# Optimization experiments

Measured on AMD Instinct MI355X. Metric: run time of the kernel, lower is better.

The kernel has to match this reference:

```python
import jax, jax.numpy as jnp
import numpy as np

EPS = 1e-5  # torch LayerNorm default


def _layernorm_hd(t, gamma, beta):
    # Normalize jointly over the last two axes (n_heads, head_dim),
    # matching nn.LayerNorm((n_heads, head_dim)).
    mu = jnp.mean(t, axis=(-2, -1), keepdims=True)
    var = jnp.var(t, axis=(-2, -1), keepdims=True)
    return (t - mu) * jax.lax.rsqrt(var + EPS) * gamma + beta


def setup_inputs() -> dict:
    key = jax.random.key(0)
    B, Hs, Ws, C = 4, 256, 256, 128  # batch, spatial grid, hidden_channels
    n_heads, head_dim = 4, C // 4
    scale = (C ** 2) / n_heads  # hidden_channels**2 / n_heads, as in __init__
    ks = jax.random.split(key, 4)
    X = jax.random.normal(ks[0], (B, Hs, Ws, C), dtype=jnp.float32)
    Wq = jax.random.normal(ks[1], (C, n_heads, head_dim), dtype=jnp.float32) / scale
    Wk = jax.random.normal(ks[2], (C, n_heads, head_dim), dtype=jnp.float32) / scale
    Wv = jax.random.normal(ks[3], (C, n_heads, head_dim), dtype=jnp.float32) / scale
    # NOTE: original forward applies layernorm_key to BOTH key and value
    # (layernorm_value params are unused); we replicate that exactly.
    gamma_k = jnp.ones((n_heads, head_dim), dtype=jnp.float32)
    beta_k = jnp.zeros((n_heads, head_dim), dtype=jnp.float32)
    return {"X": X, "Wq": Wq, "Wk": Wk, "Wv": Wv, "gamma_k": gamma_k, "beta_k": beta_k}


def reference(X, Wq, Wk, Wv, gamma_k, beta_k):
    # X: [B, Hs, Ws, C]; W*: [C, h, d]
    q = jnp.einsum('bxyc,chd->bxyhd', X, Wq)
    k = jnp.einsum('bxyc,chd->bxyhd', X, Wk)
    v = jnp.einsum('bxyc,chd->bxyhd', X, Wv)
    k = _layernorm_hd(k, gamma_k, beta_k)
    v = _layernorm_hd(v, gamma_k, beta_k)  # faithful: layernorm_key used for value too
    num_points = X.shape[1] * X.shape[2]
    kv = jnp.einsum('bxyhd,bxyhe->bhde', k, v)          # tiny [B,h,d,d]
    sa = jnp.einsum('bxyhd,bhde->bxyeh', q, kv)          # note output order (e, h)
    sa = (sa / num_points).reshape(X.shape)
    return sa
```

## Files before the change

kernel.cpp:

```cpp
#include <hip/hip_runtime.h>

#define HW 65536
#define CH 128
#define NHEADS 4
#define HDIM 32
#define EPS 1e-5f
#define INV_NP (1.0f / 65536.0f)
#define INV_C (1.0f / 128.0f)

typedef float v4f __attribute__((ext_vector_type(4)));
typedef short v8s __attribute__((ext_vector_type(8)));
typedef unsigned int v2u __attribute__((ext_vector_type(2)));
typedef unsigned int v4u __attribute__((ext_vector_type(4)));

__device__ __forceinline__ ushort f2bf(float f) {
    uint u = __float_as_uint(f);
    return (ushort)((u + 0x7FFFu + ((u >> 16) & 1u)) >> 16);
}

#define MFMA(a, b, c) __builtin_amdgcn_mfma_f32_16x16x32_bf16((a), (b), (c), 0, 0, 0)

#define LDS_WKT 0
#define LDS_WVT 16384
#define LDS_XS  32768
#define LDS_KST 32768
#define LDS_VST 36864

__global__ __launch_bounds__(256, 2) void kv_kernel(const float* __restrict__ X,
                                                    const float* __restrict__ Wk,
                                                    const float* __restrict__ Wv,
                                                    const float* __restrict__ gamma,
                                                    const float* __restrict__ beta,
                                                    float* __restrict__ kv_g) {
    __shared__ ushort lds[40960];
    const int tid  = threadIdx.x;
    const int lane = tid & 63;
    const int w    = tid >> 6;
    const int q    = lane >> 4;
    const int ln   = lane & 15;
    const int phalf = w >> 1;
    const int isv   = w & 1;
    const int WTb   = isv ? LDS_WVT : LDS_WKT;

    const int batch  = blockIdx.x >> 7;
    const int blocal = blockIdx.x & 127;
    const float* Xb = X + ((size_t)batch * HW + (size_t)blocal * 512) * CH;

#pragma unroll
    for (int n = 0; n < 16; ++n) {
        const int idx = n * 256 + tid;
        const int c  = idx >> 5;
        const int j0 = (idx & 31) << 2;
        const float4 a = ((const float4*)Wk)[idx];
        const float4 b = ((const float4*)Wv)[idx];
        const int cb = (c >> 5) * 4096 + (c & 31);
        lds[LDS_WKT + cb + (j0 + 0) * 32] = f2bf(a.x);
        lds[LDS_WKT + cb + (j0 + 1) * 32] = f2bf(a.y);
        lds[LDS_WKT + cb + (j0 + 2) * 32] = f2bf(a.z);
        lds[LDS_WKT + cb + (j0 + 3) * 32] = f2bf(a.w);
        lds[LDS_WVT + cb + (j0 + 0) * 32] = f2bf(b.x);
        lds[LDS_WVT + cb + (j0 + 1) * 32] = f2bf(b.y);
        lds[LDS_WVT + cb + (j0 + 2) * 32] = f2bf(b.z);
        lds[LDS_WVT + cb + (j0 + 3) * 32] = f2bf(b.w);
    }

    float g8[8], be8[8];
#pragma unroll
    for (int ct = 0; ct < 8; ++ct) {
        g8[ct]  = gamma[ct * 16 + ln];
        be8[ct] = beta[ct * 16 + ln];
    }

    v4f kv00 = {0.f, 0.f, 0.f, 0.f}, kv01 = kv00, kv10 = kv00, kv11 = kv00;

    float4 xp[8];
#pragma unroll
    for (int n = 0; n < 8; ++n) xp[n] = ((const float4*)Xb)[n * 256 + tid];

    for (int t = 0; t < 8; ++t) {
        __syncthreads();
#pragma unroll
        for (int n = 0; n < 8; ++n) {
            const int idx = n * 256 + tid;
            const int p  = idx >> 5;
            const int c0 = (idx & 31) << 2;
            const int off = LDS_XS + ((c0 >> 5) << 11) + (p << 5) + (c0 & 31);
            v2u pk;
            pk.x = (uint)f2bf(xp[n].x) | ((uint)f2bf(xp[n].y) << 16);
            pk.y = (uint)f2bf(xp[n].z) | ((uint)f2bf(xp[n].w) << 16);
            *(v2u*)(lds + off) = pk;
        }
        if (t < 7) {
            const float4* src = (const float4*)(Xb + (size_t)(t + 1) * 64 * CH);
#pragma unroll
            for (int n = 0; n < 8; ++n) xp[n] = src[n * 256 + tid];
        }
        __syncthreads();

        v4f acc[2][8];
#pragma unroll
        for (int rt = 0; rt < 2; ++rt)
#pragma unroll
            for (int ct = 0; ct < 8; ++ct) acc[rt][ct] = kv00 * 0.f;
#pragma unroll
        for (int ks = 0; ks < 4; ++ks) {
            const v8s A0 = *(const v8s*)(lds + LDS_XS + ks * 2048 + (phalf * 32 + ln) * 32 + q * 8);
            const v8s A1 = *(const v8s*)(lds + LDS_XS + ks * 2048 + (phalf * 32 + 16 + ln) * 32 + q * 8);
#pragma unroll
            for (int ct = 0; ct < 8; ++ct) {
                const v8s B = *(const v8s*)(lds + WTb + ks * 4096 + (ct * 16 + ln) * 32 + q * 8);
                acc[0][ct] = MFMA(A0, B, acc[0][ct]);
                acc[1][ct] = MFMA(A1, B, acc[1][ct]);
            }
        }

        float mu[2][4], rs[2][4];
#pragma unroll
        for (int rt = 0; rt < 2; ++rt) {
#pragma unroll
            for (int r = 0; r < 4; ++r) {
                float s = 0.f, sq = 0.f;
#pragma unroll
                for (int ct = 0; ct < 8; ++ct) {
                    const float v = acc[rt][ct][r];
                    s += v;
                    sq += v * v;
                }
#pragma unroll
                for (int m = 1; m <= 8; m <<= 1) {
                    s  += __shfl_xor(s, m);
                    sq += __shfl_xor(sq, m);
                }
                const float m1 = s * INV_C;
                const float var = sq * INV_C - m1 * m1;
                mu[rt][r] = m1;
                rs[rt][r] = 1.0f / sqrtf(var + EPS);
            }
        }

        __syncthreads();

#pragma unroll
        for (int rnd = 0; rnd < 2; ++rnd) {
            if (phalf == rnd) {
                const int base = (isv ? LDS_VST : LDS_KST);
#pragma unroll
                for (int ct = 0; ct < 8; ++ct) {
                    const int chb = base + (ct * 16 + ln) * 32;
#pragma unroll
                    for (int rt = 0; rt < 2; ++rt) {
#pragma unroll
                        for (int r = 0; r < 4; r += 2) {
                            const float v0 = (acc[rt][ct][r] - mu[rt][r]) * rs[rt][r] * g8[ct] + be8[ct];
                            const float v1 = (acc[rt][ct][r + 1] - mu[rt][r + 1]) * rs[rt][r + 1] * g8[ct] + be8[ct];
                            const int p32 = rt * 16 + q * 4 + r;
                            *(uint*)(lds + chb + p32) = (uint)f2bf(v0) | ((uint)f2bf(v1) << 16);
                        }
                    }
                }
            }
            __syncthreads();
            {
                const v8s Ad0 = *(const v8s*)(lds + LDS_KST + (w * 32 + ln) * 32 + q * 8);
                const v8s Ad1 = *(const v8s*)(lds + LDS_KST + (w * 32 + 16 + ln) * 32 + q * 8);
                const v8s Be0 = *(const v8s*)(lds + LDS_VST + (w * 32 + ln) * 32 + q * 8);
                const v8s Be1 = *(const v8s*)(lds + LDS_VST + (w * 32 + 16 + ln) * 32 + q * 8);
                kv00 = MFMA(Ad0, Be0, kv00);
                kv01 = MFMA(Ad0, Be1, kv01);
                kv10 = MFMA(Ad1, Be0, kv10);
                kv11 = MFMA(Ad1, Be1, kv11);
            }
            __syncthreads();
        }
    }

    float* dst = kv_g + (batch * NHEADS + w) * (HDIM * HDIM);
#pragma unroll
    for (int dt = 0; dt < 2; ++dt)
#pragma unroll
        for (int et = 0; et < 2; ++et) {
            const v4f f = dt == 0 ? (et == 0 ? kv00 : kv01) : (et == 0 ? kv10 : kv11);
#pragma unroll
            for (int r = 0; r < 4; ++r) {
                const int d = dt * 16 + q * 4 + r;
                const int e = et * 16 + ln;
                atomicAdd(&dst[d * HDIM + e], f[r]);
            }
        }
}

__global__ __launch_bounds__(256) void weff_kernel(const float* __restrict__ Wq,
                                                   const float* __restrict__ kv_g,
                                                   ushort* __restrict__ WeffT) {
    const int b = blockIdx.x >> 4;
    const int part = blockIdx.x & 15;
    const int base = part * 1024 + threadIdx.x * 4;
    const int c = base >> 7;
    const int o0 = base & 127;
    const float* kvb = kv_g + b * (NHEADS * HDIM * HDIM);
#pragma unroll
    for (int n = 0; n < 4; ++n) {
        const int o = o0 + n;
        const int h = o & 3;
        const int e = o >> 2;
        float s = 0.f;
#pragma unroll
        for (int d = 0; d < HDIM; ++d)
            s += Wq[c * CH + h * HDIM + d] * kvb[h * (HDIM * HDIM) + d * HDIM + e];
        WeffT[b * (CH * CH) + o * CH + c] = f2bf(s * INV_NP);
    }
}

__global__ __launch_bounds__(256, 2) void out_kernel(const float* __restrict__ X,
                                                     const ushort* __restrict__ WeffT,
                                                     float* __restrict__ out) {
    __shared__ ushort lds[32768];
    const int tid  = threadIdx.x;
    const int lane = tid & 63;
    const int w    = tid >> 6;
    const int q    = lane >> 4;
    const int ln   = lane & 15;
    const int phalf = w >> 1;
    const int chalf = w & 1;

    const int batch  = blockIdx.x >> 8;
    const int blocal = blockIdx.x & 255;
    const size_t p0 = (size_t)batch * HW + (size_t)blocal * 256;
    const float* Xb = X + p0 * CH;

    float4 xp[8];
#pragma unroll
    for (int n = 0; n < 8; ++n) xp[n] = ((const float4*)Xb)[n * 256 + tid];

    const ushort* Wt = WeffT + batch * (CH * CH);
#pragma unroll
    for (int n = 0; n < 8; ++n) {
        const int idx = n * 256 + tid;
        const int o  = idx >> 4;
        const int c0 = (idx & 15) << 3;
        const v4u vv = ((const v4u*)Wt)[idx];
        *(v4u*)(lds + (c0 >> 5) * 4096 + o * 32 + (c0 & 31)) = vv;
    }

#pragma unroll
    for (int n = 0; n < 8; ++n) {
        const int idx = n * 256 + tid;
        const int p  = idx >> 5;
        const int c0 = (idx & 31) << 2;
        v2u pk;
        pk.x = (uint)f2bf(xp[n].x) | ((uint)f2bf(xp[n].y) << 16);
        pk.y = (uint)f2bf(xp[n].z) | ((uint)f2bf(xp[n].w) << 16);
        *(v2u*)(lds + 16384 + ((c0 >> 5) << 11) + (p << 5) + (c0 & 31)) = pk;
    }
    __syncthreads();

    for (int t = 0; t < 4; ++t) {
        if (t < 3) {
            const float4* src = (const float4*)(Xb + (size_t)(t + 1) * 64 * CH);
#pragma unroll
            for (int n = 0; n < 8; ++n) xp[n] = src[n * 256 + tid];
        }
        const int xsb = 16384 + (t & 1) * 8192;

        v4f acc[2][4];
#pragma unroll
        for (int rt = 0; rt < 2; ++rt)
#pragma unroll
            for (int ct = 0; ct < 4; ++ct) acc[rt][ct] = (v4f){0.f, 0.f, 0.f, 0.f};
#pragma unroll
        for (int ks = 0; ks < 4; ++ks) {
            const v8s A0 = *(const v8s*)(lds + xsb + ks * 2048 + (phalf * 32 + ln) * 32 + q * 8);
            const v8s A1 = *(const v8s*)(lds + xsb + ks * 2048 + (phalf * 32 + 16 + ln) * 32 + q * 8);
#pragma unroll
            for (int ct = 0; ct < 4; ++ct) {
                const v8s B = *(const v8s*)(lds + ks * 4096 + (chalf * 64 + ct * 16 + ln) * 32 + q * 8);
                acc[0][ct] = MFMA(A0, B, acc[0][ct]);
                acc[1][ct] = MFMA(A1, B, acc[1][ct]);
            }
        }

        if (t < 3) {
            const int xsb2 = 16384 + ((t + 1) & 1) * 8192;
#pragma unroll
            for (int n = 0; n < 8; ++n) {
                const int idx = n * 256 + tid;
                const int p  = idx >> 5;
                const int c0 = (idx & 31) << 2;
                v2u pk;
                pk.x = (uint)f2bf(xp[n].x) | ((uint)f2bf(xp[n].y) << 16);
                pk.y = (uint)f2bf(xp[n].z) | ((uint)f2bf(xp[n].w) << 16);
                *(v2u*)(lds + xsb2 + ((c0 >> 5) << 11) + (p << 5) + (c0 & 31)) = pk;
            }
        }

        float* op = out + (p0 + t * 64) * CH;
#pragma unroll
        for (int rt = 0; rt < 2; ++rt)
#pragma unroll
            for (int ct = 0; ct < 4; ++ct)
#pragma unroll
                for (int r = 0; r < 4; ++r) {
                    const int p = phalf * 32 + rt * 16 + q * 4 + r;
                    const int col = chalf * 64 + ct * 16 + ln;
                    op[p * CH + col] = acc[rt][ct][r];
                }
        __syncthreads();
    }
}

extern "C" void kernel_launch(void* const* d_in, const int* in_sizes, int n_in,
                              void* d_out, int out_size, void* d_ws, size_t ws_size,
                              hipStream_t stream) {
    const float* X     = (const float*)d_in[0];
    const float* Wq    = (const float*)d_in[1];
    const float* Wk    = (const float*)d_in[2];
    const float* Wv    = (const float*)d_in[3];
    const float* gamma = (const float*)d_in[4];
    const float* beta  = (const float*)d_in[5];
    float* out = (float*)d_out;

    float*  kv_g  = (float*)d_ws;
    ushort* WeffT = (ushort*)((char*)d_ws + 65536);

    hipMemsetAsync(kv_g, 0, 16384 * sizeof(float), stream);
    kv_kernel<<<512, 256, 0, stream>>>(X, Wk, Wv, gamma, beta, kv_g);
    weff_kernel<<<64, 256, 0, stream>>>(Wq, kv_g, WeffT);
    out_kernel<<<1024, 256, 0, stream>>>(X, WeffT, out);
}
```

Before: 307.9 us.

## Load X fragments directly into registers, pre-swizzle weights, drop X LDS staging

A new prep kernel converts Wk and Wv to bf16 once, writes them in a swizzled transposed layout, and zeroes the kv accumulator, replacing the memset. The kv and out kernels now copy the pre-swizzled weights into LDS with vector copies and load X straight from global memory into MFMA A-fragments, removing the X LDS staging and several barriers. LDS layouts use XOR-style rotation to avoid bank conflicts, and out_kernel uses smaller blocks without the occupancy hint. In exchange, the explicit register prefetch of the next X tile is gone, so global load latency is now exposed, and the uncoalesced per-lane 32-byte loads may cost bandwidth.

```diff
diff --git a/kernel.cpp b/kernel.cpp
--- a/kernel.cpp
+++ b/kernel.cpp
@@ -10,7 +10,6 @@
 
 typedef float v4f __attribute__((ext_vector_type(4)));
 typedef short v8s __attribute__((ext_vector_type(8)));
-typedef unsigned int v2u __attribute__((ext_vector_type(2)));
 typedef unsigned int v4u __attribute__((ext_vector_type(4)));
 
 __device__ __forceinline__ ushort f2bf(float f) {
@@ -18,17 +17,40 @@
     return (ushort)((u + 0x7FFFu + ((u >> 16) & 1u)) >> 16);
 }
 
+__device__ __forceinline__ v8s pack8(float4 a, float4 b) {
+    v8s r;
+    r[0] = (short)f2bf(a.x); r[1] = (short)f2bf(a.y);
+    r[2] = (short)f2bf(a.z); r[3] = (short)f2bf(a.w);
+    r[4] = (short)f2bf(b.x); r[5] = (short)f2bf(b.y);
+    r[6] = (short)f2bf(b.z); r[7] = (short)f2bf(b.w);
+    return r;
+}
+
 #define MFMA(a, b, c) __builtin_amdgcn_mfma_f32_16x16x32_bf16((a), (b), (c), 0, 0, 0)
 
-#define LDS_WKT 0
-#define LDS_WVT 16384
-#define LDS_XS  32768
-#define LDS_KST 32768
-#define LDS_VST 36864
+
+__global__ __launch_bounds__(256) void prep_kernel(const float* __restrict__ Wk,
+                                                   const float* __restrict__ Wv,
+                                                   ushort* __restrict__ SWkT,
+                                                   ushort* __restrict__ SWvT,
+                                                   float* __restrict__ kv_g) {
+    const int t = blockIdx.x * 256 + threadIdx.x;
+    kv_g[t] = 0.f;
+    kv_g[t + 8192] = 0.f;
+#pragma unroll
+    for (int i = 0; i < 2; ++i) {
+        const int e = i * 8192 + t;
+        const int c = e >> 7;
+        const int row = e & 127;
+        const int dst = row * 128 + (((c >> 3) + row) & 15) * 8 + (c & 7);
+        SWkT[dst] = f2bf(Wk[e]);
+        SWvT[dst] = f2bf(Wv[e]);
+    }
+}
 
 __global__ __launch_bounds__(256, 2) void kv_kernel(const float* __restrict__ X,
-                                                    const float* __restrict__ Wk,
-                                                    const float* __restrict__ Wv,
+                                                    const ushort* __restrict__ SWkT,
+                                                    const ushort* __restrict__ SWvT,
                                                     const float* __restrict__ gamma,
                                                     const float* __restrict__ beta,
                                                     float* __restrict__ kv_g) {
@@ -40,28 +62,22 @@
     const int ln   = lane & 15;
     const int phalf = w >> 1;
     const int isv   = w & 1;
-    const int WTb   = isv ? LDS_WVT : LDS_WKT;
+    const int Wb    = isv ? 16384 : 0;
 
     const int batch  = blockIdx.x >> 7;
     const int blocal = blockIdx.x & 127;
     const float* Xb = X + ((size_t)batch * HW + (size_t)blocal * 512) * CH;
 
-#pragma unroll
-    for (int n = 0; n < 16; ++n) {
-        const int idx = n * 256 + tid;
-        const int c  = idx >> 5;
-        const int j0 = (idx & 31) << 2;
-        const float4 a = ((const float4*)Wk)[idx];
-        const float4 b = ((const float4*)Wv)[idx];
-        const int cb = (c >> 5) * 4096 + (c & 31);
-        lds[LDS_WKT + cb + (j0 + 0) * 32] = f2bf(a.x);
-        lds[LDS_WKT + cb + (j0 + 1) * 32] = f2bf(a.y);
-        lds[LDS_WKT + cb + (j0 + 2) * 32] = f2bf(a.z);
-        lds[LDS_WKT + cb + (j0 + 3) * 32] = f2bf(a.w);
-        lds[LDS_WVT + cb + (j0 + 0) * 32] = f2bf(b.x);
-        lds[LDS_WVT + cb + (j0 + 1) * 32] = f2bf(b.y);
-        lds[LDS_WVT + cb + (j0 + 2) * 32] = f2bf(b.z);
-        lds[LDS_WVT + cb + (j0 + 3) * 32] = f2bf(b.w);
+    {
+        const v4u* sk = (const v4u*)SWkT;
+        const v4u* sv = (const v4u*)SWvT;
+        v4u* dk = (v4u*)lds;
+        v4u* dv = (v4u*)(lds + 16384);
+#pragma unroll
+        for (int n = 0; n < 8; ++n) {
+            dk[n * 256 + tid] = sk[n * 256 + tid];
+            dv[n * 256 + tid] = sv[n * 256 + tid];
+        }
     }
 
     float g8[8], be8[8];
@@ -73,44 +89,40 @@
 
     v4f kv00 = {0.f, 0.f, 0.f, 0.f}, kv01 = kv00, kv10 = kv00, kv11 = kv00;
 
-    float4 xp[8];
-#pragma unroll
-    for (int n = 0; n < 8; ++n) xp[n] = ((const float4*)Xb)[n * 256 + tid];
+    __syncthreads();
 
     for (int t = 0; t < 8; ++t) {
-        __syncthreads();
-#pragma unroll
-        for (int n = 0; n < 8; ++n) {
-            const int idx = n * 256 + tid;
-            const int p  = idx >> 5;
-            const int c0 = (idx & 31) << 2;
-            const int off = LDS_XS + ((c0 >> 5) << 11) + (p << 5) + (c0 & 31);
-            v2u pk;
-            pk.x = (uint)f2bf(xp[n].x) | ((uint)f2bf(xp[n].y) << 16);
-            pk.y = (uint)f2bf(xp[n].z) | ((uint)f2bf(xp[n].w) << 16);
-            *(v2u*)(lds + off) = pk;
-        }
-        if (t < 7) {
-            const float4* src = (const float4*)(Xb + (size_t)(t + 1) * 64 * CH);
-#pragma unroll
-            for (int n = 0; n < 8; ++n) xp[n] = src[n * 256 + tid];
-        }
-        __syncthreads();
+        const float* Xt = Xb + (size_t)t * 64 * CH;
+
+        float4 xa[4][4];
+#pragma unroll
+        for (int ks = 0; ks < 4; ++ks) {
+            const float* b0 = Xt + (phalf * 32 + ln) * CH + ks * 32 + q * 8;
+            xa[ks][0] = *(const float4*)b0;
+            xa[ks][1] = *(const float4*)(b0 + 4);
+            xa[ks][2] = *(const float4*)(b0 + 16 * CH);
+            xa[ks][3] = *(const float4*)(b0 + 16 * CH + 4);
+        }
+        v8s A0[4], A1[4];
+#pragma unroll
+        for (int ks = 0; ks < 4; ++ks) {
+            A0[ks] = pack8(xa[ks][0], xa[ks][1]);
+            A1[ks] = pack8(xa[ks][2], xa[ks][3]);
+        }
 
         v4f acc[2][8];
 #pragma unroll
         for (int rt = 0; rt < 2; ++rt)
 #pragma unroll
-            for (int ct = 0; ct < 8; ++ct) acc[rt][ct] = kv00 * 0.f;
-#pragma unroll
-        for (int ks = 0; ks < 4; ++ks) {
-            const v8s A0 = *(const v8s*)(lds + LDS_XS + ks * 2048 + (phalf * 32 + ln) * 32 + q * 8);
-            const v8s A1 = *(const v8s*)(lds + LDS_XS + ks * 2048 + (phalf * 32 + 16 + ln) * 32 + q * 8);
+            for (int ct = 0; ct < 8; ++ct) acc[rt][ct] = (v4f){0.f, 0.f, 0.f, 0.f};
+#pragma unroll
+        for (int ks = 0; ks < 4; ++ks) {
 #pragma unroll
             for (int ct = 0; ct < 8; ++ct) {
-                const v8s B = *(const v8s*)(lds + WTb + ks * 4096 + (ct * 16 + ln) * 32 + q * 8);
-                acc[0][ct] = MFMA(A0, B, acc[0][ct]);
-                acc[1][ct] = MFMA(A1, B, acc[1][ct]);
+                const int row = ct * 16 + ln;
+                const v8s B = *(const v8s*)(lds + Wb + row * 128 + (((ks * 4 + q) + row) & 15) * 8);
+                acc[0][ct] = MFMA(A0[ks], B, acc[0][ct]);
+                acc[1][ct] = MFMA(A1[ks], B, acc[1][ct]);
             }
         }
 
@@ -138,15 +150,13 @@
             }
         }
 
-        __syncthreads();
-
 #pragma unroll
         for (int rnd = 0; rnd < 2; ++rnd) {
             if (phalf == rnd) {
-                const int base = (isv ? LDS_VST : LDS_KST);
+                const int base = 32768 + isv * 4096;
 #pragma unroll
                 for (int ct = 0; ct < 8; ++ct) {
-                    const int chb = base + (ct * 16 + ln) * 32;
+                    const int chn = ct * 16 + ln;
 #pragma unroll
                     for (int rt = 0; rt < 2; ++rt) {
 #pragma unroll
@@ -154,17 +164,20 @@
                             const float v0 = (acc[rt][ct][r] - mu[rt][r]) * rs[rt][r] * g8[ct] + be8[ct];
                             const float v1 = (acc[rt][ct][r + 1] - mu[rt][r + 1]) * rs[rt][r + 1] * g8[ct] + be8[ct];
                             const int p32 = rt * 16 + q * 4 + r;
-                            *(uint*)(lds + chb + p32) = (uint)f2bf(v0) | ((uint)f2bf(v1) << 16);
+                            const int off = base + chn * 32 + (((p32 >> 3) + chn) & 3) * 8 + (p32 & 7);
+                            *(uint*)(lds + off) = (uint)f2bf(v0) | ((uint)f2bf(v1) << 16);
                         }
                     }
                 }
             }
             __syncthreads();
             {
-                const v8s Ad0 = *(const v8s*)(lds + LDS_KST + (w * 32 + ln) * 32 + q * 8);
-                const v8s Ad1 = *(const v8s*)(lds + LDS_KST + (w * 32 + 16 + ln) * 32 + q * 8);
-                const v8s Be0 = *(const v8s*)(lds + LDS_VST + (w * 32 + ln) * 32 + q * 8);
-                const v8s Be1 = *(const v8s*)(lds + LDS_VST + (w * 32 + 16 + ln) * 32 + q * 8);
+                const int r0 = w * 32 + ln;
+                const int r1 = r0 + 16;
+                const v8s Ad0 = *(const v8s*)(lds + 32768 + r0 * 32 + ((q + r0) & 3) * 8);
+                const v8s Ad1 = *(const v8s*)(lds + 32768 + r1 * 32 + ((q + r1) & 3) * 8);
+                const v8s Be0 = *(const v8s*)(lds + 36864 + r0 * 32 + ((q + r0) & 3) * 8);
+                const v8s Be1 = *(const v8s*)(lds + 36864 + r1 * 32 + ((q + r1) & 3) * 8);
                 kv00 = MFMA(Ad0, Be0, kv00);
                 kv01 = MFMA(Ad0, Be1, kv01);
                 kv10 = MFMA(Ad1, Be0, kv10);
@@ -191,7 +204,7 @@
 
 __global__ __launch_bounds__(256) void weff_kernel(const float* __restrict__ Wq,
                                                    const float* __restrict__ kv_g,
-                                                   ushort* __restrict__ WeffT) {
+                                                   ushort* __restrict__ SWeffT) {
     const int b = blockIdx.x >> 4;
     const int part = blockIdx.x & 15;
     const int base = part * 1024 + threadIdx.x * 4;
@@ -207,14 +220,14 @@
 #pragma unroll
         for (int d = 0; d < HDIM; ++d)
             s += Wq[c * CH + h * HDIM + d] * kvb[h * (HDIM * HDIM) + d * HDIM + e];
-        WeffT[b * (CH * CH) + o * CH + c] = f2bf(s * INV_NP);
-    }
-}
-
-__global__ __launch_bounds__(256, 2) void out_kernel(const float* __restrict__ X,
-                                                     const ushort* __restrict__ WeffT,
-                                                     float* __restrict__ out) {
-    __shared__ ushort lds[32768];
+        SWeffT[b * (CH * CH) + o * 128 + (((c >> 3) + o) & 15) * 8 + (c & 7)] = f2bf(s * INV_NP);
+    }
+}
+
+__global__ __launch_bounds__(256) void out_kernel(const float* __restrict__ X,
+                                                  const ushort* __restrict__ SWeffT,
+                                                  float* __restrict__ out) {
+    __shared__ ushort lds[16384];
     const int tid  = threadIdx.x;
     const int lane = tid & 63;
     const int w    = tid >> 6;
@@ -223,44 +236,36 @@
     const int phalf = w >> 1;
     const int chalf = w & 1;
 
-    const int batch  = blockIdx.x >> 8;
-    const int blocal = blockIdx.x & 255;
-    const size_t p0 = (size_t)batch * HW + (size_t)blocal * 256;
-    const float* Xb = X + p0 * CH;
-
-    float4 xp[8];
-#pragma unroll
-    for (int n = 0; n < 8; ++n) xp[n] = ((const float4*)Xb)[n * 256 + tid];
-
-    const ushort* Wt = WeffT + batch * (CH * CH);
-#pragma unroll
-    for (int n = 0; n < 8; ++n) {
-        const int idx = n * 256 + tid;
-        const int o  = idx >> 4;
-        const int c0 = (idx & 15) << 3;
-        const v4u vv = ((const v4u*)Wt)[idx];
-        *(v4u*)(lds + (c0 >> 5) * 4096 + o * 32 + (c0 & 31)) = vv;
-    }
-
-#pragma unroll
-    for (int n = 0; n < 8; ++n) {
-        const int idx = n * 256 + tid;
-        const int p  = idx >> 5;
-        const int c0 = (idx & 31) << 2;
-        v2u pk;
-        pk.x = (uint)f2bf(xp[n].x) | ((uint)f2bf(xp[n].y) << 16);
-        pk.y = (uint)f2bf(xp[n].z) | ((uint)f2bf(xp[n].w) << 16);
-        *(v2u*)(lds + 16384 + ((c0 >> 5) << 11) + (p << 5) + (c0 & 31)) = pk;
+    const int batch  = blockIdx.x >> 9;
+    const int blocal = blockIdx.x & 511;
+    const size_t p0 = (size_t)batch * HW + (size_t)blocal * 128;
+
+    {
+        const v4u* s = (const v4u*)(SWeffT + batch * (CH * CH));
+        v4u* d = (v4u*)lds;
+#pragma unroll
+        for (int n = 0; n < 8; ++n) d[n * 256 + tid] = s[n * 256 + tid];
     }
     __syncthreads();
 
-    for (int t = 0; t < 4; ++t) {
-        if (t < 3) {
-            const float4* src = (const float4*)(Xb + (size_t)(t + 1) * 64 * CH);
-#pragma unroll
-            for (int n = 0; n < 8; ++n) xp[n] = src[n * 256 + tid];
-        }
-        const int xsb = 16384 + (t & 1) * 8192;
+    for (int t = 0; t < 2; ++t) {
+        const float* Xt = X + (p0 + (size_t)t * 64) * CH;
+
+        float4 xa[4][4];
+#pragma unroll
+        for (int ks = 0; ks < 4; ++ks) {
+            const float* b0 = Xt + (phalf * 32 + ln) * CH + ks * 32 + q * 8;
+            xa[ks][0] = *(const float4*)b0;
+            xa[ks][1] = *(const float4*)(b0 + 4);
+            xa[ks][2] = *(const float4*)(b0 + 16 * CH);
+            xa[ks][3] = *(const float4*)(b0 + 16 * CH + 4);
+        }
+        v8s A0[4], A1[4];
+#pragma unroll
+        for (int ks = 0; ks < 4; ++ks) {
+            A0[ks] = pack8(xa[ks][0], xa[ks][1]);
+            A1[ks] = pack8(xa[ks][2], xa[ks][3]);
+        }
 
         v4f acc[2][4];
 #pragma unroll
@@ -269,31 +274,16 @@
             for (int ct = 0; ct < 4; ++ct) acc[rt][ct] = (v4f){0.f, 0.f, 0.f, 0.f};
 #pragma unroll
         for (int ks = 0; ks < 4; ++ks) {
-            const v8s A0 = *(const v8s*)(lds + xsb + ks * 2048 + (phalf * 32 + ln) * 32 + q * 8);
-            const v8s A1 = *(const v8s*)(lds + xsb + ks * 2048 + (phalf * 32 + 16 + ln) * 32 + q * 8);
 #pragma unroll
             for (int ct = 0; ct < 4; ++ct) {
-                const v8s B = *(const v8s*)(lds + ks * 4096 + (chalf * 64 + ct * 16 + ln) * 32 + q * 8);
-                acc[0][ct] = MFMA(A0, B, acc[0][ct]);
-                acc[1][ct] = MFMA(A1, B, acc[1][ct]);
-            }
-        }
-
-        if (t < 3) {
-            const int xsb2 = 16384 + ((t + 1) & 1) * 8192;
-#pragma unroll
-            for (int n = 0; n < 8; ++n) {
-                const int idx = n * 256 + tid;
-                const int p  = idx >> 5;
-                const int c0 = (idx & 31) << 2;
-                v2u pk;
-                pk.x = (uint)f2bf(xp[n].x) | ((uint)f2bf(xp[n].y) << 16);
-                pk.y = (uint)f2bf(xp[n].z) | ((uint)f2bf(xp[n].w) << 16);
-                *(v2u*)(lds + xsb2 + ((c0 >> 5) << 11) + (p << 5) + (c0 & 31)) = pk;
-            }
-        }
-
-        float* op = out + (p0 + t * 64) * CH;
+                const int row = chalf * 64 + ct * 16 + ln;
+                const v8s B = *(const v8s*)(lds + row * 128 + (((ks * 4 + q) + row) & 15) * 8);
+                acc[0][ct] = MFMA(A0[ks], B, acc[0][ct]);
+                acc[1][ct] = MFMA(A1[ks], B, acc[1][ct]);
+            }
+        }
+
+        float* op = out + (p0 + (size_t)t * 64) * CH;
 #pragma unroll
         for (int rt = 0; rt < 2; ++rt)
 #pragma unroll
@@ -304,7 +294,6 @@
                     const int col = chalf * 64 + ct * 16 + ln;
                     op[p * CH + col] = acc[rt][ct][r];
                 }
-        __syncthreads();
     }
 }
 
@@ -319,11 +308,13 @@
     const float* beta  = (const float*)d_in[5];
     float* out = (float*)d_out;
 
-    float*  kv_g  = (float*)d_ws;
-    ushort* WeffT = (ushort*)((char*)d_ws + 65536);
-
-    hipMemsetAsync(kv_g, 0, 16384 * sizeof(float), stream);
-    kv_kernel<<<512, 256, 0, stream>>>(X, Wk, Wv, gamma, beta, kv_g);
-    weff_kernel<<<64, 256, 0, stream>>>(Wq, kv_g, WeffT);
-    out_kernel<<<1024, 256, 0, stream>>>(X, WeffT, out);
-}
+    float*  kv_g   = (float*)d_ws;
+    ushort* SWkT   = (ushort*)((char*)d_ws + 65536);
+    ushort* SWvT   = (ushort*)((char*)d_ws + 98304);
+    ushort* SWeffT = (ushort*)((char*)d_ws + 131072);
+
+    prep_kernel<<<32, 256, 0, stream>>>(Wk, Wv, SWkT, SWvT, kv_g);
+    kv_kernel<<<512, 256, 0, stream>>>(X, SWkT, SWvT, gamma, beta, kv_g);
+    weff_kernel<<<64, 256, 0, stream>>>(Wq, kv_g, SWeffT);
+    out_kernel<<<2048, 256, 0, stream>>>(X, SWeffT, out);
+}
```

Result: no change. 304.6 us (-1.1%).
